# Optimization experiments

Measured on AMD Instinct MI355X. Metric: run time of the kernel, lower is better.

## Reference

```python
import jax, jax.numpy as jnp
import numpy as np

B, S, D = 4, 2048, 1024
H, DK, DV = 16, 64, 64

def setup_inputs() -> dict:
    key = jax.random.key(0)
    ks = jax.random.split(key, 14)
    sc = 0.02
    return {
        "q": jax.random.normal(ks[0], (B, S, D), jnp.float32),
        "k": jax.random.normal(ks[1], (B, S, D), jnp.float32),
        "v": jax.random.normal(ks[2], (B, S, D), jnp.float32),
        "Wq": jax.random.normal(ks[3], (D, H * DK), jnp.float32) * sc,
        "bq": jnp.zeros((H * DK,), jnp.float32),
        "Wk": jax.random.normal(ks[4], (D, H * DK), jnp.float32) * sc,
        "bk": jnp.zeros((H * DK,), jnp.float32),
        "Wv": jax.random.normal(ks[5], (D, H * DV), jnp.float32) * sc,
        "bv": jnp.zeros((H * DV,), jnp.float32),
        "Wo": jax.random.normal(ks[6], (H * DV, D), jnp.float32) * sc,
        "bo": jnp.zeros((D,), jnp.float32),
        "gamma": jnp.ones((D,), jnp.float32),
        "beta": jnp.zeros((D,), jnp.float32),
    }

def _layer_norm(x, gamma, beta, eps=1e-5):
    mu = jnp.mean(x, axis=-1, keepdims=True)
    var = jnp.mean(jnp.square(x - mu), axis=-1, keepdims=True)
    return (x - mu) * jax.lax.rsqrt(var + eps) * gamma + beta

def reference(q, k, v, Wq, bq, Wk, bk, Wv, bv, Wo, bo, gamma, beta):
    b, lq, _ = q.shape
    lk = k.shape[1]
    # projections -> [b, h, len, d]
    Q = (q @ Wq + bq).reshape(b, lq, H, DK).transpose(0, 2, 1, 3)
    K = (k @ Wk + bk).reshape(b, lk, H, DK).transpose(0, 2, 1, 3)
    V = (v @ Wv + bv).reshape(b, lk, H, DV).transpose(0, 2, 1, 3)
    scores = jnp.einsum("bhqd,bhkd->bhqk", Q, K) / np.sqrt(DK).astype(np.float32)
    attn = jax.nn.softmax(scores, axis=-1)
    out = jnp.einsum("bhqk,bhkd->bhqd", attn, V)
    out = out.transpose(0, 2, 1, 3).reshape(b, lq, H * DV)
    out = out @ Wo + bo
    # dropout is identity in eval mode
    out = _layer_norm(out + q, gamma, beta)
    return (out, attn)
```

## Files before the change

kernel.cpp:

```cpp
#include <hip/hip_runtime.h>
#include <stdint.h>

typedef unsigned short u16;
typedef unsigned int   u32;
typedef __attribute__((ext_vector_type(8))) short bf16x8;
typedef __attribute__((ext_vector_type(4))) float f32x4;
typedef __attribute__((ext_vector_type(4))) u32   u32x4;
typedef __attribute__((ext_vector_type(2))) u32   u32x2;

#define BB 4
#define SS 2048
#define DD 1024
#define HH 16
#define QSCALE 0.18033688011112042f

__device__ __forceinline__ u16 f2b(float f){
  u32 u = __builtin_bit_cast(u32, f);
  u32 r = (u + 0x7FFFu + ((u >> 16) & 1u)) >> 16;
  return (u16)r;
}
__device__ __forceinline__ float b2f(u16 h){
  return __builtin_bit_cast(float, (u32)h << 16);
}
__device__ __forceinline__ u32 cvtpk(float lo, float hi){
  u32 r; asm("v_cvt_pk_bf16_f32 %0, %1, %2" : "=v"(r) : "v"(lo), "v"(hi)); return r;
}

__device__ __forceinline__ void gload16(const u16* g, u16* l){
  __builtin_amdgcn_global_load_lds(
      (const __attribute__((address_space(1))) void*)(uintptr_t)g,
      (__attribute__((address_space(3))) void*)(uintptr_t)l,
      16, 0, 0);
}

__global__ __launch_bounds__(256)
void cvt_bf16(const float* __restrict__ in, u16* __restrict__ out, int npack)
{
  for(int i = blockIdx.x * 256 + threadIdx.x; i < npack; i += gridDim.x * 256){
    const float4* p = (const float4*)in + 2 * (size_t)i;
    float4 a = p[0], b = p[1];
    u32x4 o;
    o.x = f2b(a.x) | ((u32)f2b(a.y) << 16);
    o.y = f2b(a.z) | ((u32)f2b(a.w) << 16);
    o.z = f2b(b.x) | ((u32)f2b(b.y) << 16);
    o.w = f2b(b.z) | ((u32)f2b(b.w) << 16);
    ((u32x4*)out)[i] = o;
  }
}

__global__ void transpose_cvt(const float* __restrict__ W, u16* __restrict__ Wt)
{
  __shared__ float tile[32][33];
  const int tx = threadIdx.x, ty = threadIdx.y;
  const int n0 = blockIdx.x * 32, k0 = blockIdx.y * 32;
  #pragma unroll
  for(int j = 0; j < 4; ++j)
    tile[ty + j*8][tx] = W[(size_t)(k0 + ty + j*8) * DD + n0 + tx];
  __syncthreads();
  #pragma unroll
  for(int j = 0; j < 4; ++j)
    Wt[(size_t)(n0 + ty + j*8) * DD + k0 + tx] = f2b(tile[tx][ty + j*8]);
}

template<int MODE>
__global__ __launch_bounds__(256)
void gemm128(const u16* __restrict__ A, const u16* __restrict__ Bt,
             const float* __restrict__ bias, void* __restrict__ Cout)
{
  __shared__ __align__(16) u16 As[128*32];
  __shared__ __align__(16) u16 Bs[128*32];
  const int tid = threadIdx.x;
  const int w = tid >> 6, ln = tid & 63, g = ln >> 4, c16 = ln & 15;
  const int m0 = blockIdx.y * 128, n0 = blockIdx.x * 128;
  const int wr = (w >> 1) * 64, wc = (w & 1) * 64;

  f32x4 acc[4][4] = {};

  for(int kt = 0; kt < 1024; kt += 32){
    __syncthreads();
    {
      const int f0 = w * 2;
      #pragma unroll
      for(int j = 0; j < 2; ++j){
        int e = ((f0 + j) * 64 + ln) * 8;
        gload16(Bt + (size_t)(n0 + (e >> 5)) * 1024 + kt + (e & 31),
                Bs + (size_t)(f0 + j) * 512);
        gload16(A + (size_t)(m0 + (e >> 5)) * 1024 + kt + (e & 31),
                As + (size_t)(f0 + j) * 512);
      }
    }
    __syncthreads();
    bf16x8 a[4], b[4];
    #pragma unroll
    for(int mi = 0; mi < 4; ++mi)
      a[mi] = *(const bf16x8*)(As + (wr + mi*16 + c16) * 32 + g * 8);
    #pragma unroll
    for(int ni = 0; ni < 4; ++ni)
      b[ni] = *(const bf16x8*)(Bs + (wc + ni*16 + c16) * 32 + g * 8);
    #pragma unroll
    for(int mi = 0; mi < 4; ++mi)
      #pragma unroll
      for(int ni = 0; ni < 4; ++ni)
        acc[mi][ni] = __builtin_amdgcn_mfma_f32_16x16x32_bf16(a[mi], b[ni], acc[mi][ni], 0, 0, 0);
  }

  #pragma unroll
  for(int ni = 0; ni < 4; ++ni){
    const int colg = n0 + wc + ni*16 + c16;
    const float bv = bias[colg];
    #pragma unroll
    for(int mi = 0; mi < 4; ++mi){
      #pragma unroll
      for(int e = 0; e < 4; ++e){
        const int rowg = m0 + wr + mi*16 + g*4 + e;
        float val = acc[mi][ni][e] + bv;
        const int bb = rowg >> 11, s = rowg & 2047, h = colg >> 6, d = colg & 63;
        if (MODE == 0){
          val *= QSCALE;
          ((u16*)Cout)[((size_t)(bb*HH + h) * SS + s) * 64 + d] = f2b(val);
        } else if (MODE == 1){
          ((u16*)Cout)[((size_t)(bb*HH + h) * SS + s) * 64 + d] = f2b(val);
        } else if (MODE == 2){
          ((u16*)Cout)[((size_t)(bb*HH + h) * 64 + d) * SS + s] = f2b(val);
        } else {
          ((float*)Cout)[(size_t)rowg * 1024 + colg] = val;
        }
      }
    }
  }
}

__global__ __launch_bounds__(256)
void attn7(const u16* __restrict__ Qb, const u16* __restrict__ Kb,
           const u16* __restrict__ Vt, float* __restrict__ attn_out,
           u16* __restrict__ AO)
{
  __shared__ __align__(16) u16 Ks[3][64*64];
  __shared__ __align__(16) u16 Vs[3][64*64];
  __shared__ __align__(16) u16 pbuf[4][2][16*64];
  const int tid = threadIdx.x, w = tid >> 6, ln = tid & 63, g = ln >> 4, c = ln & 15;
  const int bh = blockIdx.y;
  const int q0 = blockIdx.x * 128 + w * 32;

  const u16* Qp = Qb + ((size_t)bh * SS + q0) * 64;
  const u16* Kp = Kb + (size_t)bh * SS * 64;
  const u16* Vp = Vt + (size_t)bh * 64 * SS;

  const bf16x8 bq00 = *(const bf16x8*)(Qp + c * 64 + g * 8);
  const bf16x8 bq01 = *(const bf16x8*)(Qp + c * 64 + 32 + g * 8);
  const bf16x8 bq10 = *(const bf16x8*)(Qp + (16 + c) * 64 + g * 8);
  const bf16x8 bq11 = *(const bf16x8*)(Qp + (16 + c) * 64 + 32 + g * 8);

  auto stageK = [&](int slot, int t){
    const u16* src = Kp + (size_t)t * 64 * 64;
    #pragma unroll
    for(int j = 0; j < 2; ++j){
      int idx = j * 256 + tid;
      int r = idx >> 3, s5 = idx & 7;
      gload16(src + r * 64 + (((s5 ^ (r & 7))) << 3), &Ks[slot][idx << 3]);
    }
  };
  auto stageV = [&](int slot, int t){
    #pragma unroll
    for(int j = 0; j < 2; ++j){
      int idx = j * 256 + tid;
      int r = idx >> 3, s5 = idx & 7;
      gload16(Vp + (size_t)r * SS + t * 64 + (((s5 ^ (r & 7))) << 3), &Vs[slot][idx << 3]);
    }
  };

  float l0 = 0.f, l1 = 0.f;
  stageK(0, 0); stageK(1, 1);
  asm volatile("s_waitcnt vmcnt(2)" ::: "memory");
  __builtin_amdgcn_s_barrier();
  for(int t = 0; t < 32; ++t){
    if(t < 30) stageK((t + 2) % 3, t + 2);
    __builtin_amdgcn_sched_barrier(0);
    const u16* kb_ = &Ks[t % 3][0];
    f32x4 s[2][4] = {};
    #pragma unroll
    for(int ch = 0; ch < 4; ++ch){
      const int r = ch * 16 + c;
      bf16x8 ka0 = *(const bf16x8*)(kb_ + r * 64 + ((g       ^ (c & 7)) << 3));
      bf16x8 ka1 = *(const bf16x8*)(kb_ + r * 64 + (((4 + g) ^ (c & 7)) << 3));
      s[0][ch] = __builtin_amdgcn_mfma_f32_16x16x32_bf16(ka0, bq00, s[0][ch], 0, 0, 0);
      s[0][ch] = __builtin_amdgcn_mfma_f32_16x16x32_bf16(ka1, bq01, s[0][ch], 0, 0, 0);
      s[1][ch] = __builtin_amdgcn_mfma_f32_16x16x32_bf16(ka0, bq10, s[1][ch], 0, 0, 0);
      s[1][ch] = __builtin_amdgcn_mfma_f32_16x16x32_bf16(ka1, bq11, s[1][ch], 0, 0, 0);
    }
    #pragma unroll
    for(int ch = 0; ch < 4; ++ch)
      #pragma unroll
      for(int e = 0; e < 4; ++e){
        l0 += __builtin_amdgcn_exp2f(s[0][ch][e]);
        l1 += __builtin_amdgcn_exp2f(s[1][ch][e]);
      }
    if(t < 30)       asm volatile("s_waitcnt vmcnt(2)" ::: "memory");
    else if(t == 30) asm volatile("s_waitcnt vmcnt(0)" ::: "memory");
    __builtin_amdgcn_s_barrier();
  }
  l0 += __shfl_xor(l0, 16, 64); l0 += __shfl_xor(l0, 32, 64);
  l1 += __shfl_xor(l1, 16, 64); l1 += __shfl_xor(l1, 32, 64);
  const float rl0 = 1.f / l0, rl1 = 1.f / l1;

  f32x4 acc[2][4] = {};
  float* aout = attn_out + ((size_t)bh * SS + q0) * SS;
  u16* pw0 = &pbuf[w][0][0];
  u16* pw1 = &pbuf[w][1][0];

  stageK(0, 0); stageV(0, 0); stageK(1, 1); stageV(1, 1);
  asm volatile("s_waitcnt vmcnt(4)" ::: "memory");
  __builtin_amdgcn_s_barrier();

  for(int t = 0; t < 32; ++t){
    if(t < 30){ stageK((t + 2) % 3, t + 2); stageV((t + 2) % 3, t + 2); }
    __builtin_amdgcn_sched_barrier(0);
    const int kv0 = t * 64;
    const u16* kb_ = &Ks[t % 3][0];
    const u16* vb_ = &Vs[t % 3][0];

    f32x4 s[2][4] = {};
    __builtin_amdgcn_s_setprio(1);
    #pragma unroll
    for(int ch = 0; ch < 4; ++ch){
      const int r = ch * 16 + c;
      bf16x8 ka0 = *(const bf16x8*)(kb_ + r * 64 + ((g       ^ (c & 7)) << 3));
      bf16x8 ka1 = *(const bf16x8*)(kb_ + r * 64 + (((4 + g) ^ (c & 7)) << 3));
      s[0][ch] = __builtin_amdgcn_mfma_f32_16x16x32_bf16(ka0, bq00, s[0][ch], 0, 0, 0);
      s[0][ch] = __builtin_amdgcn_mfma_f32_16x16x32_bf16(ka1, bq01, s[0][ch], 0, 0, 0);
      s[1][ch] = __builtin_amdgcn_mfma_f32_16x16x32_bf16(ka0, bq10, s[1][ch], 0, 0, 0);
      s[1][ch] = __builtin_amdgcn_mfma_f32_16x16x32_bf16(ka1, bq11, s[1][ch], 0, 0, 0);
    }
    __builtin_amdgcn_s_setprio(0);

    #pragma unroll
    for(int qb = 0; qb < 2; ++qb){
      const float rl = qb ? rl1 : rl0;
      u16* pw = qb ? pw1 : pw0;
      #pragma unroll
      for(int ch = 0; ch < 4; ++ch){
        float p0 = __builtin_amdgcn_exp2f(s[qb][ch][0]) * rl;
        float p1 = __builtin_amdgcn_exp2f(s[qb][ch][1]) * rl;
        float p2 = __builtin_amdgcn_exp2f(s[qb][ch][2]) * rl;
        float p3 = __builtin_amdgcn_exp2f(s[qb][ch][3]) * rl;
        u32x2 pk2 = { cvtpk(p0, p1), cvtpk(p2, p3) };
        *(u32x2*)((char*)pw + c * 128 + (((ch * 2 + (g >> 1)) ^ (c & 7)) << 4) + ((g & 1) << 3)) = pk2;
      }
    }
    asm volatile("s_waitcnt lgkmcnt(0)" ::: "memory");
    __builtin_amdgcn_sched_barrier(0);

    __builtin_amdgcn_s_setprio(1);
    #pragma unroll
    for(int kc = 0; kc < 2; ++kc){
      bf16x8 ap0 = *(const bf16x8*)((const char*)pw0 + c * 128 + (((kc * 4 + g) ^ (c & 7)) << 4));
      bf16x8 ap1 = *(const bf16x8*)((const char*)pw1 + c * 128 + (((kc * 4 + g) ^ (c & 7)) << 4));
      #pragma unroll
      for(int ni = 0; ni < 4; ++ni){
        bf16x8 bv = *(const bf16x8*)(vb_ + (ni * 16 + c) * 64 + (((kc * 4 + g) ^ (c & 7)) << 3));
        acc[0][ni] = __builtin_amdgcn_mfma_f32_16x16x32_bf16(ap0, bv, acc[0][ni], 0, 0, 0);
        acc[1][ni] = __builtin_amdgcn_mfma_f32_16x16x32_bf16(ap1, bv, acc[1][ni], 0, 0, 0);
      }
    }
    __builtin_amdgcn_s_setprio(0);

    {
      const int r8 = ln >> 3;
      const int jl = ln & 7;
      #pragma unroll
      for(int qb = 0; qb < 2; ++qb){
        const u16* pw = qb ? pw1 : pw0;
        #pragma unroll
        for(int rh = 0; rh < 2; ++rh){
          const int r = rh * 8 + r8;
          #pragma unroll
          for(int chf = 0; chf < 2; ++chf){
            const int jg = chf * 8 + jl;
            const int ch2 = jg >> 2, g2 = jg & 3;
            const int slot = ch2 * 2 + (g2 >> 1);
            u32x2 pk = *(const u32x2*)((const char*)pw + r * 128 +
                         (((slot ^ (r & 7))) << 4) + ((g2 & 1) << 3));
            f32x4 o;
            o[0] = b2f((u16)(pk.x & 0xFFFFu)); o[1] = b2f((u16)(pk.x >> 16));
            o[2] = b2f((u16)(pk.y & 0xFFFFu)); o[3] = b2f((u16)(pk.y >> 16));
            *(f32x4*)(aout + (size_t)(qb * 16 + r) * SS + kv0 + jg * 4) = o;
          }
        }
      }
    }

    if(t == 0)       asm volatile("s_waitcnt vmcnt(12)" ::: "memory");
    else if(t < 30)  asm volatile("s_waitcnt vmcnt(20)" ::: "memory");
    else if(t == 30) asm volatile("s_waitcnt vmcnt(16)" ::: "memory");
    __builtin_amdgcn_s_barrier();
  }

  u16* aos = &pbuf[w][0][0];
  #pragma unroll
  for(int qb = 0; qb < 2; ++qb)
    #pragma unroll
    for(int ni = 0; ni < 4; ++ni)
      #pragma unroll
      for(int e = 0; e < 4; ++e)
        aos[(qb * 16 + 4 * g + e) * 64 + ni * 16 + c] = f2b(acc[qb][ni][e]);
  asm volatile("s_waitcnt lgkmcnt(0)" ::: "memory");
  __builtin_amdgcn_sched_barrier(0);
  {
    const int bb = bh >> 4, h = bh & 15;
    #pragma unroll
    for(int p2 = 0; p2 < 4; ++p2){
      int idx = p2 * 64 + ln;
      int row = idx >> 3, col16 = (idx & 7) * 8;
      u16* dst = AO + ((size_t)bb * SS + q0 + row) * 1024 + h * 64 + col16;
      *(u32x4*)dst = *(const u32x4*)(aos + row * 64 + col16);
    }
  }
}

__global__ __launch_bounds__(256)
void ln_kernel(const float* __restrict__ tmp, const float* __restrict__ qin,
               const float* __restrict__ gamma, const float* __restrict__ beta,
               float* __restrict__ out)
{
  __shared__ float rs[4], rs2[4];
  const int row = blockIdx.x, tid = threadIdx.x;
  const int w = tid >> 6, ln = tid & 63;
  const float4 x4 = *(const float4*)(tmp + (size_t)row * 1024 + tid * 4);
  const float4 q4 = *(const float4*)(qin + (size_t)row * 1024 + tid * 4);
  const float xs0 = x4.x + q4.x, xs1 = x4.y + q4.y, xs2 = x4.z + q4.z, xs3 = x4.w + q4.w;
  float s  = xs0 + xs1 + xs2 + xs3;
  float s2 = xs0*xs0 + xs1*xs1 + xs2*xs2 + xs3*xs3;
  #pragma unroll
  for(int m = 1; m < 64; m <<= 1){
    s  += __shfl_xor(s,  m, 64);
    s2 += __shfl_xor(s2, m, 64);
  }
  if(ln == 0){ rs[w] = s; rs2[w] = s2; }
  __syncthreads();
  s  = rs[0]  + rs[1]  + rs[2]  + rs[3];
  s2 = rs2[0] + rs2[1] + rs2[2] + rs2[3];
  const float mu   = s * (1.f / 1024.f);
  const float var  = s2 * (1.f / 1024.f) - mu * mu;
  const float rstd = rsqrtf(var + 1e-5f);
  const float4 g4 = *(const float4*)(gamma + tid * 4);
  const float4 b4 = *(const float4*)(beta + tid * 4);
  float4 o;
  o.x = (xs0 - mu) * rstd * g4.x + b4.x;
  o.y = (xs1 - mu) * rstd * g4.y + b4.y;
  o.z = (xs2 - mu) * rstd * g4.z + b4.z;
  o.w = (xs3 - mu) * rstd * g4.w + b4.w;
  *(float4*)(out + (size_t)row * 1024 + tid * 4) = o;
}

extern "C" void kernel_launch(void* const* d_in, const int* in_sizes, int n_in,
                              void* d_out, int out_size, void* d_ws, size_t ws_size,
                              hipStream_t stream)
{
  (void)in_sizes; (void)n_in; (void)out_size; (void)ws_size;
  const float* q     = (const float*)d_in[0];
  const float* k     = (const float*)d_in[1];
  const float* v     = (const float*)d_in[2];
  const float* Wq    = (const float*)d_in[3];
  const float* bq    = (const float*)d_in[4];
  const float* Wk    = (const float*)d_in[5];
  const float* bk    = (const float*)d_in[6];
  const float* Wv    = (const float*)d_in[7];
  const float* bv    = (const float*)d_in[8];
  const float* Wo    = (const float*)d_in[9];
  const float* bo    = (const float*)d_in[10];
  const float* gamma = (const float*)d_in[11];
  const float* beta  = (const float*)d_in[12];

  char* p = (char*)d_ws;
  auto alloc = [&](size_t bytes) -> void* {
    void* r = (void*)p; p += (bytes + 255) & ~(size_t)255; return r;
  };
  const size_t NTOK = (size_t)BB * SS;
  u16* WtQ  = (u16*)alloc((size_t)DD * DD * 2);
  u16* WtK  = (u16*)alloc((size_t)DD * DD * 2);
  u16* WtV  = (u16*)alloc((size_t)DD * DD * 2);
  u16* WtO  = (u16*)alloc((size_t)DD * DD * 2);
  u16* Qb   = (u16*)alloc(NTOK * DD * 2);
  u16* Kb   = (u16*)alloc(NTOK * DD * 2);
  u16* Vtb  = (u16*)alloc(NTOK * DD * 2);
  u16* AO   = (u16*)alloc(NTOK * DD * 2);
  u16* qbf  = (u16*)alloc(NTOK * DD * 2);
  u16* kbf  = (u16*)alloc(NTOK * DD * 2);
  u16* vbf  = (u16*)alloc(NTOK * DD * 2);
  float* tmp = (float*)alloc(NTOK * DD * 4);

  float* out0 = (float*)d_out;
  float* attn = out0 + NTOK * DD;

  const int NPACK = (int)(NTOK * DD / 8);
  cvt_bf16<<<dim3(2048), 256, 0, stream>>>(q, qbf, NPACK);
  cvt_bf16<<<dim3(2048), 256, 0, stream>>>(k, kbf, NPACK);
  cvt_bf16<<<dim3(2048), 256, 0, stream>>>(v, vbf, NPACK);

  const dim3 tb(32, 8);
  transpose_cvt<<<dim3(32, 32), tb, 0, stream>>>(Wq, WtQ);
  transpose_cvt<<<dim3(32, 32), tb, 0, stream>>>(Wk, WtK);
  transpose_cvt<<<dim3(32, 32), tb, 0, stream>>>(Wv, WtV);
  transpose_cvt<<<dim3(32, 32), tb, 0, stream>>>(Wo, WtO);

  gemm128<0><<<dim3(8, 64), 256, 0, stream>>>(qbf, WtQ, bq, Qb);
  gemm128<1><<<dim3(8, 64), 256, 0, stream>>>(kbf, WtK, bk, Kb);
  gemm128<2><<<dim3(8, 64), 256, 0, stream>>>(vbf, WtV, bv, Vtb);

  attn7<<<dim3(16, 64), 256, 0, stream>>>(Qb, Kb, Vtb, attn, AO);

  gemm128<3><<<dim3(8, 64), 256, 0, stream>>>(AO, WtO, bo, tmp);
  ln_kernel<<<dim3(8192), 256, 0, stream>>>(tmp, q, gamma, beta, out0);
}
```

Before: 486.3 us.

## Batch projection launches and stage GEMM epilogues through LDS for coalesced stores

Merges the three input conversions, the four weight transposes and the three QKV projection GEMMs into single launches, each selecting its operands by grid z/y index. This cuts launch count and lets blocks from different projections share the machine. The GEMM epilogues now stage results in swizzled shared memory and write 16-byte vectors, replacing scattered 2-byte stores. This matters most for the transposed V output, which previously wrote with a stride of SS. The cost is larger LDS usage (32KB per block) and extra LDS traffic in the epilogue.

Result: faster. 471.5 us (-3.0%).

```diff
diff --git a/kernel.cpp b/kernel.cpp
--- a/kernel.cpp
+++ b/kernel.cpp
@@ -34,8 +34,12 @@
 }
 
 __global__ __launch_bounds__(256)
-void cvt_bf16(const float* __restrict__ in, u16* __restrict__ out, int npack)
-{
+void cvt_bf16_3(const float* __restrict__ q, const float* __restrict__ k,
+                const float* __restrict__ v, u16* __restrict__ qo,
+                u16* __restrict__ ko, u16* __restrict__ vo, int npack)
+{
+  const float* in = blockIdx.y == 0 ? q : (blockIdx.y == 1 ? k : v);
+  u16* out        = blockIdx.y == 0 ? qo : (blockIdx.y == 1 ? ko : vo);
   for(int i = blockIdx.x * 256 + threadIdx.x; i < npack; i += gridDim.x * 256){
     const float4* p = (const float4*)in + 2 * (size_t)i;
     float4 a = p[0], b = p[1];
@@ -48,8 +52,13 @@
   }
 }
 
-__global__ void transpose_cvt(const float* __restrict__ W, u16* __restrict__ Wt)
-{
+__global__ void transpose_cvt4(const float* __restrict__ W0, const float* __restrict__ W1,
+                               const float* __restrict__ W2, const float* __restrict__ W3,
+                               u16* __restrict__ T0, u16* __restrict__ T1,
+                               u16* __restrict__ T2, u16* __restrict__ T3)
+{
+  const float* W = blockIdx.z == 0 ? W0 : (blockIdx.z == 1 ? W1 : (blockIdx.z == 2 ? W2 : W3));
+  u16*        Wt = blockIdx.z == 0 ? T0 : (blockIdx.z == 1 ? T1 : (blockIdx.z == 2 ? T2 : T3));
   __shared__ float tile[32][33];
   const int tx = threadIdx.x, ty = threadIdx.y;
   const int n0 = blockIdx.x * 32, k0 = blockIdx.y * 32;
@@ -62,13 +71,21 @@
     Wt[(size_t)(n0 + ty + j*8) * DD + k0 + tx] = f2b(tile[tx][ty + j*8]);
 }
 
-template<int MODE>
 __global__ __launch_bounds__(256)
-void gemm128(const u16* __restrict__ A, const u16* __restrict__ Bt,
-             const float* __restrict__ bias, void* __restrict__ Cout)
-{
-  __shared__ __align__(16) u16 As[128*32];
-  __shared__ __align__(16) u16 Bs[128*32];
+void gemm_qkv(const u16* __restrict__ qA, const u16* __restrict__ kA, const u16* __restrict__ vA,
+              const u16* __restrict__ BtQ, const u16* __restrict__ BtK, const u16* __restrict__ BtV,
+              const float* __restrict__ bq, const float* __restrict__ bk, const float* __restrict__ bv,
+              u16* __restrict__ Qo, u16* __restrict__ Ko, u16* __restrict__ Vo)
+{
+  const int mode = blockIdx.z;
+  const u16* A   = mode == 0 ? qA  : (mode == 1 ? kA  : vA);
+  const u16* Bt  = mode == 0 ? BtQ : (mode == 1 ? BtK : BtV);
+  const float* bias = mode == 0 ? bq : (mode == 1 ? bk : bv);
+  u16* Cout      = mode == 0 ? Qo  : (mode == 1 ? Ko  : Vo);
+
+  __shared__ __align__(16) u16 smem[16384];
+  u16* As = smem;
+  u16* Bs = smem + 128*32;
   const int tid = threadIdx.x;
   const int w = tid >> 6, ln = tid & 63, g = ln >> 4, c16 = ln & 15;
   const int m0 = blockIdx.y * 128, n0 = blockIdx.x * 128;
@@ -103,30 +120,133 @@
       for(int ni = 0; ni < 4; ++ni)
         acc[mi][ni] = __builtin_amdgcn_mfma_f32_16x16x32_bf16(a[mi], b[ni], acc[mi][ni], 0, 0, 0);
   }
-
+  __syncthreads();
+
+  char* st = (char*)smem + w * 8192;
+  const float sc = (mode == 0) ? QSCALE : 1.f;
+  const int bb = m0 >> 11;
+  const int h  = (n0 + wc) >> 6;
+  const int sbase = (m0 + wr) & 2047;
+
+  if(mode < 2){
+    #pragma unroll
+    for(int ni = 0; ni < 4; ++ni){
+      const float bvv = bias[n0 + wc + ni*16 + c16];
+      const int gr = ni*2 + (c16 >> 3);
+      const int within = (c16 & 7) * 2;
+      #pragma unroll
+      for(int mi = 0; mi < 4; ++mi)
+        #pragma unroll
+        for(int e = 0; e < 4; ++e){
+          const int row = mi*16 + g*4 + e;
+          *(u16*)(st + row*128 + ((gr ^ (row & 7)) << 4) + within)
+              = f2b((acc[mi][ni][e] + bvv) * sc);
+        }
+    }
+    asm volatile("s_waitcnt lgkmcnt(0)" ::: "memory");
+    const int r8 = ln >> 3, jl = ln & 7;
+    #pragma unroll
+    for(int ii = 0; ii < 8; ++ii){
+      const int row = ii*8 + r8;
+      u16* dst = Cout + (((size_t)(bb*HH + h) * SS) + sbase + row) * 64 + jl*8;
+      *(u32x4*)dst = *(const u32x4*)(st + row*128 + ((jl ^ (row & 7)) << 4));
+    }
+  } else {
+    #pragma unroll
+    for(int ni = 0; ni < 4; ++ni){
+      const float bvv = bias[n0 + wc + ni*16 + c16];
+      const int row = ni*16 + c16;
+      #pragma unroll
+      for(int mi = 0; mi < 4; ++mi)
+        #pragma unroll
+        for(int e = 0; e < 4; ++e){
+          const int sl = mi*16 + g*4 + e;
+          const int gr = sl >> 3;
+          *(u16*)(st + row*128 + ((gr ^ (row & 7)) << 4) + (sl & 7) * 2)
+              = f2b(acc[mi][ni][e] + bvv);
+        }
+    }
+    asm volatile("s_waitcnt lgkmcnt(0)" ::: "memory");
+    const int r8 = ln >> 3, jl = ln & 7;
+    #pragma unroll
+    for(int ii = 0; ii < 8; ++ii){
+      const int d = ii*8 + r8;
+      u16* dst = Cout + ((size_t)(bb*HH + h) * 64 + (n0 + wc - ((n0+wc)>>6<<6)) + d) * SS + sbase + jl*8;
+      *(u32x4*)dst = *(const u32x4*)(st + d*128 + ((jl ^ (d & 7)) << 4));
+    }
+  }
+}
+
+__global__ __launch_bounds__(256)
+void gemm_o(const u16* __restrict__ A, const u16* __restrict__ Bt,
+            const float* __restrict__ bias, float* __restrict__ Cout)
+{
+  __shared__ __align__(16) u16 smem[16384];
+  u16* As = smem;
+  u16* Bs = smem + 128*32;
+  const int tid = threadIdx.x;
+  const int w = tid >> 6, ln = tid & 63, g = ln >> 4, c16 = ln & 15;
+  const int m0 = blockIdx.y * 128, n0 = blockIdx.x * 128;
+  const int wr = (w >> 1) * 64, wc = (w & 1) * 64;
+
+  f32x4 acc[4][4] = {};
+
+  for(int kt = 0; kt < 1024; kt += 32){
+    __syncthreads();
+    {
+      const int f0 = w * 2;
+      #pragma unroll
+      for(int j = 0; j < 2; ++j){
+        int e = ((f0 + j) * 64 + ln) * 8;
+        gload16(Bt + (size_t)(n0 + (e >> 5)) * 1024 + kt + (e & 31),
+                Bs + (size_t)(f0 + j) * 512);
+        gload16(A + (size_t)(m0 + (e >> 5)) * 1024 + kt + (e & 31),
+                As + (size_t)(f0 + j) * 512);
+      }
+    }
+    __syncthreads();
+    bf16x8 a[4], b[4];
+    #pragma unroll
+    for(int mi = 0; mi < 4; ++mi)
+      a[mi] = *(const bf16x8*)(As + (wr + mi*16 + c16) * 32 + g * 8);
+    #pragma unroll
+    for(int ni = 0; ni < 4; ++ni)
+      b[ni] = *(const bf16x8*)(Bs + (wc + ni*16 + c16) * 32 + g * 8);
+    #pragma unroll
+    for(int mi = 0; mi < 4; ++mi)
+      #pragma unroll
+      for(int ni = 0; ni < 4; ++ni)
+        acc[mi][ni] = __builtin_amdgcn_mfma_f32_16x16x32_bf16(a[mi], b[ni], acc[mi][ni], 0, 0, 0);
+  }
+  __syncthreads();
+
+  char* st = (char*)smem + w * 8192;
+  const int r8 = ln >> 3, jl = ln & 7;
   #pragma unroll
-  for(int ni = 0; ni < 4; ++ni){
-    const int colg = n0 + wc + ni*16 + c16;
-    const float bv = bias[colg];
-    #pragma unroll
-    for(int mi = 0; mi < 4; ++mi){
-      #pragma unroll
-      for(int e = 0; e < 4; ++e){
-        const int rowg = m0 + wr + mi*16 + g*4 + e;
-        float val = acc[mi][ni][e] + bv;
-        const int bb = rowg >> 11, s = rowg & 2047, h = colg >> 6, d = colg & 63;
-        if (MODE == 0){
-          val *= QSCALE;
-          ((u16*)Cout)[((size_t)(bb*HH + h) * SS + s) * 64 + d] = f2b(val);
-        } else if (MODE == 1){
-          ((u16*)Cout)[((size_t)(bb*HH + h) * SS + s) * 64 + d] = f2b(val);
-        } else if (MODE == 2){
-          ((u16*)Cout)[((size_t)(bb*HH + h) * 64 + d) * SS + s] = f2b(val);
-        } else {
-          ((float*)Cout)[(size_t)rowg * 1024 + colg] = val;
+  for(int half = 0; half < 2; ++half){
+    #pragma unroll
+    for(int ni2 = 0; ni2 < 2; ++ni2){
+      const int ni = half*2 + ni2;
+      const float bvv = bias[n0 + wc + ni*16 + c16];
+      const int gr = ni2*4 + (c16 >> 2);
+      const int within = (c16 & 3) * 4;
+      #pragma unroll
+      for(int mi = 0; mi < 4; ++mi)
+        #pragma unroll
+        for(int e = 0; e < 4; ++e){
+          const int row = mi*16 + g*4 + e;
+          *(float*)(st + row*128 + ((gr ^ (row & 7)) << 4) + within)
+              = acc[mi][ni][e] + bvv;
         }
-      }
-    }
+    }
+    asm volatile("s_waitcnt lgkmcnt(0)" ::: "memory");
+    #pragma unroll
+    for(int ii = 0; ii < 8; ++ii){
+      const int row = ii*8 + r8;
+      float* dst = Cout + (size_t)(m0 + wr + row) * 1024 + n0 + wc + half*32 + jl*4;
+      *(f32x4*)dst = *(const f32x4*)(st + row*128 + ((jl ^ (row & 7)) << 4));
+    }
+    asm volatile("s_waitcnt lgkmcnt(0)" ::: "memory");
   }
 }
 
@@ -393,22 +513,16 @@
   float* attn = out0 + NTOK * DD;
 
   const int NPACK = (int)(NTOK * DD / 8);
-  cvt_bf16<<<dim3(2048), 256, 0, stream>>>(q, qbf, NPACK);
-  cvt_bf16<<<dim3(2048), 256, 0, stream>>>(k, kbf, NPACK);
-  cvt_bf16<<<dim3(2048), 256, 0, stream>>>(v, vbf, NPACK);
-
-  const dim3 tb(32, 8);
-  transpose_cvt<<<dim3(32, 32), tb, 0, stream>>>(Wq, WtQ);
-  transpose_cvt<<<dim3(32, 32), tb, 0, stream>>>(Wk, WtK);
-  transpose_cvt<<<dim3(32, 32), tb, 0, stream>>>(Wv, WtV);
-  transpose_cvt<<<dim3(32, 32), tb, 0, stream>>>(Wo, WtO);
-
-  gemm128<0><<<dim3(8, 64), 256, 0, stream>>>(qbf, WtQ, bq, Qb);
-  gemm128<1><<<dim3(8, 64), 256, 0, stream>>>(kbf, WtK, bk, Kb);
-  gemm128<2><<<dim3(8, 64), 256, 0, stream>>>(vbf, WtV, bv, Vtb);
+  cvt_bf16_3<<<dim3(1024, 3), 256, 0, stream>>>(q, k, v, qbf, kbf, vbf, NPACK);
+
+  transpose_cvt4<<<dim3(32, 32, 4), dim3(32, 8), 0, stream>>>(
+      Wq, Wk, Wv, Wo, WtQ, WtK, WtV, WtO);
+
+  gemm_qkv<<<dim3(8, 64, 3), 256, 0, stream>>>(
+      qbf, kbf, vbf, WtQ, WtK, WtV, bq, bk, bv, Qb, Kb, Vtb);
 
   attn7<<<dim3(16, 64), 256, 0, stream>>>(Qb, Kb, Vtb, attn, AO);
 
-  gemm128<3><<<dim3(8, 64), 256, 0, stream>>>(AO, WtO, bo, tmp);
+  gemm_o<<<dim3(8, 64), 256, 0, stream>>>(AO, WtO, bo, tmp);
   ln_kernel<<<dim3(8192), 256, 0, stream>>>(tmp, q, gamma, beta, out0);
 }
```
